# Kernel tuning notes

Hardware: AMD Instinct MI355X
Metric: run time of the kernel (lower is better)

The kernel has to match this reference:

```python
import jax, jax.numpy as jnp
import numpy as np

PRE_NMS_TOPN = 6000   # cfg.TEST.RPN_PRE_NMS_TOP_N
POST_NMS_TOPN = 1000  # cfg.TEST.RPN_POST_NMS_TOP_N
NMS_THRESH = 0.7      # cfg.TEST.RPN_NMS_THRESH
MIN_SIZE = 0.0        # cfg.TEST.RPN_MIN_SIZE
BBOX_XFORM_CLIP = float(np.log(1000.0 / 16.0))
FEAT_STRIDE = 8.0     # 1 / spatial_scale


def _generate_anchors(base_size=16, ratios=(0.5, 1.0, 2.0), scales=(2, 4, 8, 16, 32)):
    """Standard Detectron anchor generation -> (A, 4) = (15, 4)."""
    def whctrs(a):
        w = a[2] - a[0] + 1.0
        h = a[3] - a[1] + 1.0
        return w, h, a[0] + 0.5 * (w - 1.0), a[1] + 0.5 * (h - 1.0)

    def mk(ws, hs, xc, yc):
        ws = ws[:, None]; hs = hs[:, None]
        return np.hstack([xc - 0.5 * (ws - 1.0), yc - 0.5 * (hs - 1.0),
                          xc + 0.5 * (ws - 1.0), yc + 0.5 * (hs - 1.0)])

    base = np.array([0.0, 0.0, base_size - 1.0, base_size - 1.0])
    w, h, xc, yc = whctrs(base)
    rs = np.array(ratios)
    ws = np.round(np.sqrt(w * h / rs))
    hs = np.round(ws * rs)
    ratio_anchors = mk(ws, hs, xc, yc)
    out = []
    for a in ratio_anchors:
        w, h, xc, yc = whctrs(a)
        sc = np.array(scales, dtype=np.float64)
        out.append(mk(w * sc, h * sc, xc, yc))
    return np.vstack(out).astype(np.float32)


def _proposals_one_image(all_anchors, im_info, bbox_deltas, scores):
    # bbox_deltas: (4A, H, W), scores: (A, H, W)
    deltas = bbox_deltas.transpose(1, 2, 0).reshape(-1, 4)  # (K*A, 4)
    s = scores.transpose(1, 2, 0).reshape(-1)               # (K*A,)

    # pre-NMS top-k by objectness (argpartition+argsort in original)
    top_s, order = jax.lax.top_k(s, PRE_NMS_TOPN)
    d = deltas[order]
    anc = all_anchors[order]

    # bbox_transform with weights (1,1,1,1) and dw/dh clipping
    ws = anc[:, 2] - anc[:, 0] + 1.0
    hs = anc[:, 3] - anc[:, 1] + 1.0
    cx = anc[:, 0] + 0.5 * ws
    cy = anc[:, 1] + 0.5 * hs
    dx, dy = d[:, 0], d[:, 1]
    dw = jnp.minimum(d[:, 2], BBOX_XFORM_CLIP)
    dh = jnp.minimum(d[:, 3], BBOX_XFORM_CLIP)
    pcx = dx * ws + cx
    pcy = dy * hs + cy
    pw = jnp.exp(dw) * ws
    ph = jnp.exp(dh) * hs
    x1 = pcx - 0.5 * pw
    y1 = pcy - 0.5 * ph
    x2 = pcx + 0.5 * pw - 1.0
    y2 = pcy + 0.5 * ph - 1.0

    # clip_tiled_boxes to image extent
    h_im, w_im, scale = im_info[0], im_info[1], im_info[2]
    x1 = jnp.clip(x1, 0.0, w_im - 1.0)
    y1 = jnp.clip(y1, 0.0, h_im - 1.0)
    x2 = jnp.clip(x2, 0.0, w_im - 1.0)
    y2 = jnp.clip(y2, 0.0, h_im - 1.0)
    boxes = jnp.stack([x1, y1, x2, y2], axis=1)  # (PRE, 4)

    # _filter_boxes -> validity mask (replaces gather-by-keep)
    bws = x2 - x1 + 1.0
    bhs = y2 - y1 + 1.0
    min_sz = MIN_SIZE * scale
    valid = (bws >= min_sz) & (bhs >= min_sz) & ((x1 + bws / 2.0) < w_im) & ((y1 + bhs / 2.0) < h_im)

    # greedy NMS on score-sorted boxes (boxes already sorted descending)
    areas = bws * bhs
    ix1 = jnp.maximum(x1[:, None], x1[None, :])
    iy1 = jnp.maximum(y1[:, None], y1[None, :])
    ix2 = jnp.minimum(x2[:, None], x2[None, :])
    iy2 = jnp.minimum(y2[:, None], y2[None, :])
    inter = jnp.maximum(ix2 - ix1 + 1.0, 0.0) * jnp.maximum(iy2 - iy1 + 1.0, 0.0)
    iou = inter / (areas[:, None] + areas[None, :] - inter)

    later = jnp.arange(PRE_NMS_TOPN)

    def body(i, keep):
        sup = keep[i] & (iou[i] > NMS_THRESH) & (later > i)
        return keep & ~sup

    keep = jax.lax.fori_loop(0, PRE_NMS_TOPN, body, valid)

    # fixed-size output: top POST_NMS_TOPN surviving boxes, padded (score=-1, box=0)
    masked = jnp.where(keep, top_s, -1.0)
    out_s, idx = jax.lax.top_k(masked, POST_NMS_TOPN)
    pad = (out_s > -1.0).astype(boxes.dtype)
    out_b = boxes[idx] * pad[:, None]
    return out_b, out_s


def reference(rpn_cls_prob, rpn_bbox_pred, im_info, anchors):
    N, A, H, W = rpn_cls_prob.shape
    dt = rpn_bbox_pred.dtype
    shift_x = jnp.arange(W, dtype=dt) * FEAT_STRIDE
    shift_y = jnp.arange(H, dtype=dt) * FEAT_STRIDE
    # torch.meshgrid default 'ij' ordering (faithful to original)
    sx, sy = jnp.meshgrid(shift_x, shift_y, indexing='ij')  # (W, H)
    shifts = jnp.stack([sx.ravel(), sy.ravel(), sx.ravel(), sy.ravel()], axis=1)  # (K, 4)
    all_anchors = (anchors[None, :, :] + shifts[:, None, :]).reshape(-1, 4)  # (K*A, 4)

    boxes, probs = jax.vmap(_proposals_one_image, in_axes=(None, 0, 0, 0))(
        all_anchors, im_info, rpn_bbox_pred, rpn_cls_prob)
    batch_inds = jnp.broadcast_to(jnp.arange(N, dtype=boxes.dtype)[:, None, None],
                                  (N, POST_NMS_TOPN, 1))
    rois = jnp.concatenate([batch_inds, boxes], axis=-1).reshape(-1, 5)
    return rois, probs.reshape(-1)


def setup_inputs() -> dict:
    key = jax.random.key(0)
    k1, k2 = jax.random.split(key)
    N, A, H, W = 2, 15, 128, 128
    rpn_cls_prob = jax.random.uniform(k1, (N, A, H, W), dtype=jnp.float32)
    rpn_bbox_pred = jax.random.normal(k2, (N, 4 * A, H, W), dtype=jnp.float32) * 0.2
    im_info = jnp.tile(jnp.array([[1024.0, 1024.0, 1.0]], dtype=jnp.float32), (N, 1))
    anchors = jnp.asarray(_generate_anchors())
    return {"rpn_cls_prob": rpn_cls_prob, "rpn_bbox_pred": rpn_bbox_pred,
            "im_info": im_info, "anchors": anchors}
```

## Files before the change

kernel.cpp:

```cpp
#include <hip/hip_runtime.h>
#include <hip/hip_bf16.h>

#define A_NUM 15
#define HDIM 128
#define WDIM 128
#define HW (HDIM*WDIM)
#define PER_IMG (A_NUM*HW)
#define NIMG 2
#define PRE_N 6000
#define POST_N 1000
#define NBLK 94
#define NPAD (NBLK*64)
#define SORTN 8192
#define CHUNK4 4096
#define NBIN 16384
#define HPART 16

typedef unsigned long long ull;

#define META_OFF   0u
#define HIST_OFF   64u
#define SEL_OFF    131136u
#define BOX_OFF    262208u
#define VALID_OFF  550976u
#define DIAG_OFF   599104u
#define MASK_OFF   695360u

__device__ __forceinline__ unsigned int f2ord(float f) {
    unsigned int u = __float_as_uint(f);
    return (u & 0x80000000u) ? ~u : (u | 0x80000000u);
}
__device__ __forceinline__ float ord2f(unsigned int u) {
    unsigned int s = (u & 0x80000000u) ? (u ^ 0x80000000u) : ~u;
    return __uint_as_float(s);
}

__global__ __launch_bounds__(1024) void k_hist16(const float* __restrict__ cls,
                                                 unsigned int* __restrict__ hist) {
    __shared__ unsigned int h[NBIN];
    int img = blockIdx.y, part = blockIdx.x;
    int t = threadIdx.x;
    for (int b = t; b < NBIN; b += 1024) h[b] = 0;
    __syncthreads();
    int base = img * PER_IMG + part * (PER_IMG / HPART);
    for (int e = t; e < PER_IMG / HPART; e += 1024) {
        unsigned int u = f2ord(cls[base + e]);
        unsigned int bin = (u >> 16) - 0x8000u;
        if (bin > (NBIN - 1)) bin = NBIN - 1;
        atomicAdd(&h[bin], 1u);
    }
    __syncthreads();
    unsigned int* hp = hist + (size_t)img * NBIN;
    for (int b = t; b < NBIN; b += 1024)
        if (h[b]) atomicAdd(&hp[b], h[b]);
}

__global__ __launch_bounds__(1024) void k_scan16(const unsigned int* __restrict__ hist,
                                                 unsigned int* __restrict__ meta) {
    __shared__ unsigned int csum[1024];
    __shared__ unsigned int aux[64];
    __shared__ unsigned int binv[16];
    int img = blockIdx.x, t = threadIdx.x;
    const unsigned int* hp = hist + (size_t)img * NBIN;
    unsigned int s = 0;
    #pragma unroll
    for (int q = 0; q < 16; ++q) s += hp[t * 16 + q];
    csum[t] = s;
    __syncthreads();
    if (t < 64) {
        unsigned int x = 0;
        #pragma unroll
        for (int q = 0; q < 16; ++q) x += csum[t * 16 + q];
        aux[t] = x;
    }
    __syncthreads();
    if (t < 64) {
        unsigned int suf = 0;
        for (int q = t; q < 64; ++q) suf += aux[q];
        ull mb1 = __ballot(suf >= PRE_N);
        int sstar = 63 - __clzll(mb1);
        unsigned int sufnext = (unsigned)__shfl((int)suf, (sstar + 1) & 63);
        unsigned int cumAbove = (sstar == 63) ? 0u : sufnext;
        unsigned int sufC = 0;
        if (t < 16) {
            for (int q = sstar * 16 + t; q < sstar * 16 + 16; ++q) sufC += csum[q];
            sufC += cumAbove;
        }
        ull mb2 = __ballot((t < 16) && (sufC >= PRE_N));
        int crel = 63 - __clzll(mb2);
        int cstar = sstar * 16 + crel;
        unsigned int cumAbove2 = (crel == 15) ? cumAbove : (unsigned)__shfl((int)sufC, crel + 1);
        if (t < 16) binv[t] = hp[cstar * 16 + t];
        unsigned int sufB = 0;
        if (t < 16) {
            for (int q = t; q < 16; ++q) sufB += binv[q];
            sufB += cumAbove2;
        }
        ull mb3 = __ballot((t < 16) && (sufB >= PRE_N));
        int brel = 63 - __clzll(mb3);
        if (t == 0) {
            meta[2 + img] = (unsigned)(cstar * 16 + brel) + 0x8000u;
            meta[img] = 0u;
        }
    }
}

__global__ __launch_bounds__(256) void k_gather(const float* __restrict__ cls,
                                                unsigned int* __restrict__ meta,
                                                ull* __restrict__ selkeys) {
    __shared__ unsigned int lcnt[NIMG], lbase[NIMG];
    int t = threadIdx.x;
    int tid = blockIdx.x * 256 + t;
    if (t < NIMG) lcnt[t] = 0;
    __syncthreads();
    unsigned int T0 = meta[2], T1 = meta[3];
    int a = tid / HW;
    int pos = tid - a * HW;
    int m = pos * A_NUM + a;
    int lane = t & 63;
    unsigned int uv[NIMG];
    bool pr[NIMG];
    unsigned int lofs[NIMG];
    #pragma unroll
    for (int img = 0; img < NIMG; ++img) {
        unsigned int T = img ? T1 : T0;
        unsigned int u = f2ord(cls[img * PER_IMG + tid]);
        uv[img] = u;
        bool pred = (u >> 16) >= T;
        pr[img] = pred;
        ull mball = __ballot((int)pred);
        unsigned int o = 0;
        if (pred) {
            int leader = __ffsll((long long)mball) - 1;
            unsigned int wbase = 0;
            if (lane == leader) wbase = atomicAdd(&lcnt[img], (unsigned)__popcll(mball));
            wbase = (unsigned)__shfl((int)wbase, leader);
            o = wbase + (unsigned)__popcll(mball & ((1ull << lane) - 1ull));
        }
        lofs[img] = o;
    }
    __syncthreads();
    if (t < NIMG) lbase[t] = atomicAdd(&meta[t], lcnt[t]);
    __syncthreads();
    #pragma unroll
    for (int img = 0; img < NIMG; ++img) {
        if (pr[img]) {
            unsigned int p = lbase[img] + lofs[img];
            if (p < SORTN)
                selkeys[(size_t)img * SORTN + p] =
                    ((ull)(~uv[img]) << 32) | (unsigned int)m;
        }
    }
}

__global__ __launch_bounds__(512) void k_sortA(ull* __restrict__ selkeys,
                                               const unsigned int* __restrict__ meta) {
    __shared__ ull key[CHUNK4];
    int img = blockIdx.x >> 1, c = blockIdx.x & 1;
    unsigned int cnt = meta[img];
    if (cnt > SORTN) cnt = SORTN;
    ull* g = selkeys + (size_t)img * SORTN;
    int base = c * CHUNK4;
    for (int i = threadIdx.x; i < CHUNK4; i += 512)
        key[i] = (base + i < (int)cnt) ? g[base + i] : ~0ull;
    __syncthreads();
    bool desc = (c & 1);
    for (int k = 2; k <= CHUNK4; k <<= 1) {
        for (int j = k >> 1; j > 0; j >>= 1) {
            for (int p = threadIdx.x; p < CHUNK4 / 2; p += 512) {
                int i = ((p & ~(j - 1)) << 1) | (p & (j - 1));
                int x = i | j;
                bool up = (((i & k) == 0) != desc);
                ull A = key[i], B = key[x];
                if ((A > B) == up) { key[i] = B; key[x] = A; }
            }
            __syncthreads();
        }
    }
    for (int i = threadIdx.x; i < CHUNK4; i += 512) g[base + i] = key[i];
}

__global__ __launch_bounds__(512) void k_sortC(ull* __restrict__ selkeys) {
    __shared__ ull key[SORTN];
    int img = blockIdx.x;
    ull* g = selkeys + (size_t)img * SORTN;
    for (int i = threadIdx.x; i < SORTN; i += 512) key[i] = g[i];
    __syncthreads();
    for (int j = SORTN / 2; j > 0; j >>= 1) {
        for (int p = threadIdx.x; p < SORTN / 2; p += 512) {
            int i = ((p & ~(j - 1)) << 1) | (p & (j - 1));
            int x = i | j;
            ull A = key[i], B = key[x];
            if (A > B) { key[i] = B; key[x] = A; }
        }
        __syncthreads();
    }
    for (int i = threadIdx.x; i < PRE_N; i += 512) g[i] = key[i];
}

__global__ void k_decode(const ull* __restrict__ selkeys,
                         const float* __restrict__ bbox, const float* __restrict__ anchors,
                         const float* __restrict__ iminfo,
                         float* __restrict__ boxsoa, unsigned int* __restrict__ validArr) {
    int r = blockIdx.x * blockDim.x + threadIdx.x;
    int img = blockIdx.y;
    if (r >= PRE_N) return;
    ull keyv = selkeys[(size_t)img * SORTN + r];
    unsigned int m = (unsigned int)(keyv & 0xFFFFFFFFu);
    unsigned int u = ~(unsigned int)(keyv >> 32);
    float score = ord2f(u);
    int q = m / A_NUM;
    int a = m - q * A_NUM;
    int w = q & (WDIM - 1);
    int h = q >> 7;
    float sx = (float)h * 8.0f;
    float sy = (float)w * 8.0f;
    float a0 = __fadd_rn(anchors[a * 4 + 0], sx);
    float a1 = __fadd_rn(anchors[a * 4 + 1], sy);
    float a2 = __fadd_rn(anchors[a * 4 + 2], sx);
    float a3 = __fadd_rn(anchors[a * 4 + 3], sy);
    float ws = __fadd_rn(__fsub_rn(a2, a0), 1.0f);
    float hs = __fadd_rn(__fsub_rn(a3, a1), 1.0f);
    float cx = __fadd_rn(a0, __fmul_rn(0.5f, ws));
    float cy = __fadd_rn(a1, __fmul_rn(0.5f, hs));
    const float* bb = bbox + (size_t)img * 4 * A_NUM * HW;
    int base = h * WDIM + w;
    float dx = bb[(a * 4 + 0) * HW + base];
    float dy = bb[(a * 4 + 1) * HW + base];
    float dwv = bb[(a * 4 + 2) * HW + base];
    float dhv = bb[(a * 4 + 3) * HW + base];
    const float CLIPV = 4.135166556742356f;
    float dw = fminf(dwv, CLIPV);
    float dh = fminf(dhv, CLIPV);
    float pcx = __fadd_rn(__fmul_rn(dx, ws), cx);
    float pcy = __fadd_rn(__fmul_rn(dy, hs), cy);
    float pw = __fmul_rn(expf(dw), ws);
    float ph = __fmul_rn(expf(dh), hs);
    float x1 = __fsub_rn(pcx, __fmul_rn(0.5f, pw));
    float y1 = __fsub_rn(pcy, __fmul_rn(0.5f, ph));
    float x2 = __fsub_rn(__fadd_rn(pcx, __fmul_rn(0.5f, pw)), 1.0f);
    float y2 = __fsub_rn(__fadd_rn(pcy, __fmul_rn(0.5f, ph)), 1.0f);
    float him = iminfo[img * 3 + 0], wim = iminfo[img * 3 + 1], scale = iminfo[img * 3 + 2];
    float wmax = __fsub_rn(wim, 1.0f), hmax = __fsub_rn(him, 1.0f);
    x1 = fminf(fmaxf(x1, 0.0f), wmax);
    y1 = fminf(fmaxf(y1, 0.0f), hmax);
    x2 = fminf(fmaxf(x2, 0.0f), wmax);
    y2 = fminf(fmaxf(y2, 0.0f), hmax);
    float bws = __fadd_rn(__fsub_rn(x2, x1), 1.0f);
    float bhs = __fadd_rn(__fsub_rn(y2, y1), 1.0f);
    float minsz = __fmul_rn(0.0f, scale);
    bool valid = (bws >= minsz) && (bhs >= minsz) &&
                 (__fadd_rn(x1, __fdiv_rn(bws, 2.0f)) < wim) &&
                 (__fadd_rn(y1, __fdiv_rn(bhs, 2.0f)) < him);
    float area = __fmul_rn(bws, bhs);
    boxsoa[(0 * NIMG + img) * NPAD + r] = x1;
    boxsoa[(1 * NIMG + img) * NPAD + r] = y1;
    boxsoa[(2 * NIMG + img) * NPAD + r] = x2;
    boxsoa[(3 * NIMG + img) * NPAD + r] = y2;
    boxsoa[(4 * NIMG + img) * NPAD + r] = area;
    boxsoa[(5 * NIMG + img) * NPAD + r] = score;
    validArr[img * NPAD + r] = valid ? 1u : 0u;
}

__global__ __launch_bounds__(256) void k_mask(const float* __restrict__ boxsoa,
                                              ull* __restrict__ M,
                                              ull* __restrict__ diagArr) {
    int jb = blockIdx.x, ibq = blockIdx.y, img = blockIdx.z;
    if (jb < (ibq << 2)) return;
    int t = threadIdx.x, wv = t >> 6, lane = t & 63;
    __shared__ float jx1[64], jy1[64], jx2[64], jy2[64], jar[64];
    const float* X1 = boxsoa + (0 * NIMG + img) * NPAD;
    const float* Y1 = boxsoa + (1 * NIMG + img) * NPAD;
    const float* X2 = boxsoa + (2 * NIMG + img) * NPAD;
    const float* Y2 = boxsoa + (3 * NIMG + img) * NPAD;
    const float* AR = boxsoa + (4 * NIMG + img) * NPAD;
    int j0 = jb * 64;
    if (t < 64) {
        int jidx = j0 + t;
        bool jin = jidx < PRE_N;
        jx1[t] = jin ? X1[jidx] : 0.0f;
        jy1[t] = jin ? Y1[jidx] : 0.0f;
        jx2[t] = jin ? X2[jidx] : 0.0f;
        jy2[t] = jin ? Y2[jidx] : 0.0f;
        jar[t] = jin ? AR[jidx] : 1.0f;
    }
    __syncthreads();
    int ib = ibq * 4 + wv;
    if (ib >= NBLK || jb < ib) return;
    int i = ib * 64 + lane;
    ull bits = 0ULL;
    if (i < PRE_N) {
        float x1 = X1[i], y1 = Y1[i], x2 = X2[i], y2 = Y2[i], ai = AR[i];
        for (int jj = 0; jj < 64; ++jj) {
            int j = j0 + jj;
            if (j == i || j >= PRE_N) continue;
            float ix1 = fmaxf(x1, jx1[jj]);
            float iy1 = fmaxf(y1, jy1[jj]);
            float ix2 = fminf(x2, jx2[jj]);
            float iy2 = fminf(y2, jy2[jj]);
            float iw = fmaxf(__fadd_rn(__fsub_rn(ix2, ix1), 1.0f), 0.0f);
            float ih = fmaxf(__fadd_rn(__fsub_rn(iy2, iy1), 1.0f), 0.0f);
            float inter = __fmul_rn(iw, ih);
            float denom = __fsub_rn(__fadd_rn(ai, jar[jj]), inter);
            float iou = __fdiv_rn(inter, denom);
            if (iou > 0.7f) bits |= (1ULL << jj);
        }
    }
    M[((size_t)img * NPAD + (size_t)i) * NBLK + jb] = bits;
    if (jb == ib) diagArr[(size_t)img * NPAD + i] = bits;
}

__global__ __launch_bounds__(64, 1) void k_reduce(const ull* __restrict__ M_,
                                                  const ull* __restrict__ diagArr,
                                                  const unsigned int* __restrict__ validArr,
                                                  const float* __restrict__ boxsoa,
                                                  float* __restrict__ out) {
    int img = blockIdx.x;
    int t = threadIdx.x;
    __shared__ unsigned short s_list[POST_N];
    const ull* M = M_ + (size_t)img * NPAD * NBLK;
    const ull* D = diagArr + (size_t)img * NPAD;
    const unsigned int* V = validArr + img * NPAD;
    ull d_cur = D[t];
    unsigned int vraw = V[t];
    ull A_acc = 0ULL, tile_cur = 0ULL, keptb_prev = 0ULL;
    int cnt = 0;
    for (int ib = 0; ib < NBLK; ++ib) {
        int cnt_pre = cnt;
        ull a_nx0 = 0, a_nx1 = 0, a_nx2 = 0, a_nx3 = 0, a_nx4 = 0, a_nx5 = 0, a_nx6 = 0, a_nx7 = 0;
        ull a_nx8 = 0, a_nx9 = 0, a_nxA = 0, a_nxB = 0, a_nxC = 0, a_nxD = 0, a_nxE = 0, a_nxF = 0;
        ull tile_nx = 0ULL, d_nx = 0ULL;
        unsigned int v_nx = 0u;
        int col = ib + 1;
        if (col < NBLK) {
            #define AG(reg, u2) { int q = t + (u2 << 6); \
                if (q < cnt_pre) reg = M[(size_t)s_list[q] * NBLK + col]; }
            AG(a_nx0, 0) AG(a_nx1, 1) AG(a_nx2, 2) AG(a_nx3, 3)
            AG(a_nx4, 4) AG(a_nx5, 5) AG(a_nx6, 6) AG(a_nx7, 7)
            AG(a_nx8, 8) AG(a_nx9, 9) AG(a_nxA, 10) AG(a_nxB, 11)
            AG(a_nxC, 12) AG(a_nxD, 13) AG(a_nxE, 14) AG(a_nxF, 15)
            #undef AG
            tile_nx = M[(size_t)(ib * 64 + t) * NBLK + col];
            int i2 = col * 64 + t;
            d_nx = D[i2];
            v_nx = V[i2];
        }
        ull partial = A_acc | (((keptb_prev >> t) & 1ULL) ? tile_cur : 0ULL);
        unsigned int lo = (unsigned)partial, hi = (unsigned)(partial >> 32);
        #pragma unroll
        for (int s2 = 1; s2 < 64; s2 <<= 1) {
            lo |= (unsigned)__shfl_xor((int)lo, s2);
            hi |= (unsigned)__shfl_xor((int)hi, s2);
        }
        ull sup = ((ull)hi << 32) | lo;
        int i = ib * 64 + t;
        bool v_cur = (i < PRE_N) && (vraw != 0u);
        ull validw = __ballot((int)v_cur);
        ull live = validw & ~sup;
        unsigned int dlo = (unsigned)d_cur, dhi = (unsigned)(d_cur >> 32);
        ull keptb = 0ULL;
        while (live) {
            int b = __ffsll((long long)live) - 1;
            keptb |= 1ULL << b;
            if (t == 0) s_list[cnt] = (unsigned short)(ib * 64 + b);
            ++cnt;
            if (cnt >= POST_N) break;
            unsigned int rl = (unsigned)__builtin_amdgcn_readlane((int)dlo, b);
            unsigned int rh = (unsigned)__builtin_amdgcn_readlane((int)dhi, b);
            live &= ~(((ull)rh << 32) | rl);
            live &= ~(1ULL << b);
        }
        if (cnt >= POST_N) break;
        A_acc = (((a_nx0 | a_nx1) | (a_nx2 | a_nx3)) | ((a_nx4 | a_nx5) | (a_nx6 | a_nx7)))
              | (((a_nx8 | a_nx9) | (a_nxA | a_nxB)) | ((a_nxC | a_nxD) | (a_nxE | a_nxF)));
        tile_cur = tile_nx;
        d_cur = d_nx;
        vraw = v_nx;
        keptb_prev = keptb;
    }
    int total = cnt > POST_N ? POST_N : cnt;
    for (int k = t; k < POST_N; k += 64) {
        float x1 = 0.0f, y1 = 0.0f, x2 = 0.0f, y2 = 0.0f, sc = -1.0f;
        if (k < total) {
            int r = (int)s_list[k];
            x1 = boxsoa[(0 * NIMG + img) * NPAD + r];
            y1 = boxsoa[(1 * NIMG + img) * NPAD + r];
            x2 = boxsoa[(2 * NIMG + img) * NPAD + r];
            y2 = boxsoa[(3 * NIMG + img) * NPAD + r];
            sc = boxsoa[(5 * NIMG + img) * NPAD + r];
        }
        float* roi = out + (size_t)(img * POST_N + k) * 5;
        roi[0] = (float)img;
        roi[1] = x1;
        roi[2] = y1;
        roi[3] = x2;
        roi[4] = y2;
        out[NIMG * POST_N * 5 + img * POST_N + k] = sc;
    }
}

extern "C" void kernel_launch(void* const* d_in, const int* in_sizes, int n_in,
                              void* d_out, int out_size, void* d_ws, size_t ws_size,
                              hipStream_t stream) {
    const float* cls = (const float*)d_in[0];
    const float* bbox = (const float*)d_in[1];
    const float* iminfo = (const float*)d_in[2];
    const float* anchors = (const float*)d_in[3];
    float* out = (float*)d_out;
    char* ws = (char*)d_ws;

    unsigned int* meta = (unsigned int*)(ws + META_OFF);
    unsigned int* hist = (unsigned int*)(ws + HIST_OFF);
    ull* selkeys = (ull*)(ws + SEL_OFF);
    float* boxsoa = (float*)(ws + BOX_OFF);
    unsigned int* validArr = (unsigned int*)(ws + VALID_OFF);
    ull* diagArr = (ull*)(ws + DIAG_OFF);
    ull* mask = (ull*)(ws + MASK_OFF);

    hipMemsetAsync(hist, 0, (size_t)NIMG * NBIN * sizeof(unsigned int), stream);
    k_hist16<<<dim3(HPART, NIMG), 1024, 0, stream>>>(cls, hist);
    k_scan16<<<NIMG, 1024, 0, stream>>>(hist, meta);
    k_gather<<<PER_IMG / 256, 256, 0, stream>>>(cls, meta, selkeys);
    k_sortA<<<2 * NIMG, 512, 0, stream>>>(selkeys, meta);
    k_sortC<<<NIMG, 512, 0, stream>>>(selkeys);
    k_decode<<<dim3((PRE_N + 255) / 256, NIMG), 256, 0, stream>>>(selkeys, bbox, anchors, iminfo,
                                                                  boxsoa, validArr);
    k_mask<<<dim3(NBLK, (NBLK + 3) / 4, NIMG), 256, 0, stream>>>(boxsoa, mask, diagArr);
    k_reduce<<<NIMG, 64, 0, stream>>>(mask, diagArr, validArr, boxsoa, out);
}
```

Measured before the change: 292.9 us.

## Store NMS mask column-major and OR suppression via per-lane kept bitmaps

```diff
diff --git a/kernel.cpp b/kernel.cpp
--- a/kernel.cpp
+++ b/kernel.cpp
@@ -263,10 +263,10 @@
 }
 
 __global__ __launch_bounds__(256) void k_mask(const float* __restrict__ boxsoa,
-                                              ull* __restrict__ M,
+                                              ull* __restrict__ Mc,
                                               ull* __restrict__ diagArr) {
-    int jb = blockIdx.x, ibq = blockIdx.y, img = blockIdx.z;
-    if (jb < (ibq << 2)) return;
+    int cb = blockIdx.x, rbq = blockIdx.y, img = blockIdx.z;
+    if ((rbq << 2) > cb) return;
     int t = threadIdx.x, wv = t >> 6, lane = t & 63;
     __shared__ float jx1[64], jy1[64], jx2[64], jy2[64], jar[64];
     const float* X1 = boxsoa + (0 * NIMG + img) * NPAD;
@@ -274,7 +274,7 @@
     const float* X2 = boxsoa + (2 * NIMG + img) * NPAD;
     const float* Y2 = boxsoa + (3 * NIMG + img) * NPAD;
     const float* AR = boxsoa + (4 * NIMG + img) * NPAD;
-    int j0 = jb * 64;
+    int j0 = cb * 64;
     if (t < 64) {
         int jidx = j0 + t;
         bool jin = jidx < PRE_N;
@@ -285,15 +285,15 @@
         jar[t] = jin ? AR[jidx] : 1.0f;
     }
     __syncthreads();
-    int ib = ibq * 4 + wv;
-    if (ib >= NBLK || jb < ib) return;
-    int i = ib * 64 + lane;
+    int rb = rbq * 4 + wv;
+    if (rb > cb) return;
+    int r = rb * 64 + lane;
     ull bits = 0ULL;
-    if (i < PRE_N) {
-        float x1 = X1[i], y1 = Y1[i], x2 = X2[i], y2 = Y2[i], ai = AR[i];
+    if (r < PRE_N) {
+        float x1 = X1[r], y1 = Y1[r], x2 = X2[r], y2 = Y2[r], ai = AR[r];
         for (int jj = 0; jj < 64; ++jj) {
             int j = j0 + jj;
-            if (j == i || j >= PRE_N) continue;
+            if (j == r || j >= PRE_N) continue;
             float ix1 = fmaxf(x1, jx1[jj]);
             float iy1 = fmaxf(y1, jy1[jj]);
             float ix2 = fminf(x2, jx2[jj]);
@@ -306,11 +306,11 @@
             if (iou > 0.7f) bits |= (1ULL << jj);
         }
     }
-    M[((size_t)img * NPAD + (size_t)i) * NBLK + jb] = bits;
-    if (jb == ib) diagArr[(size_t)img * NPAD + i] = bits;
-}
-
-__global__ __launch_bounds__(64, 1) void k_reduce(const ull* __restrict__ M_,
+    Mc[((size_t)img * NBLK + cb) * NPAD + r] = bits;
+    if (rb == cb) diagArr[(size_t)img * NPAD + r] = bits;
+}
+
+__global__ __launch_bounds__(64, 1) void k_reduce(const ull* __restrict__ Mc,
                                                   const ull* __restrict__ diagArr,
                                                   const unsigned int* __restrict__ validArr,
                                                   const float* __restrict__ boxsoa,
@@ -318,35 +318,31 @@
     int img = blockIdx.x;
     int t = threadIdx.x;
     __shared__ unsigned short s_list[POST_N];
-    const ull* M = M_ + (size_t)img * NPAD * NBLK;
+    const ull* MC = Mc + (size_t)img * NBLK * NPAD;
     const ull* D = diagArr + (size_t)img * NPAD;
     const unsigned int* V = validArr + img * NPAD;
     ull d_cur = D[t];
     unsigned int vraw = V[t];
-    ull A_acc = 0ULL, tile_cur = 0ULL, keptb_prev = 0ULL;
+    ull kTlo = 0ULL, kThi = 0ULL;
+    ull acc_cur = 0ULL;
     int cnt = 0;
     for (int ib = 0; ib < NBLK; ++ib) {
-        int cnt_pre = cnt;
-        ull a_nx0 = 0, a_nx1 = 0, a_nx2 = 0, a_nx3 = 0, a_nx4 = 0, a_nx5 = 0, a_nx6 = 0, a_nx7 = 0;
-        ull a_nx8 = 0, a_nx9 = 0, a_nxA = 0, a_nxB = 0, a_nxC = 0, a_nxD = 0, a_nxE = 0, a_nxF = 0;
-        ull tile_nx = 0ULL, d_nx = 0ULL;
+        int col = ib + 1;
+        bool doload = col < NBLK;
+        const ull* Mcol = MC + (size_t)col * NPAD;
+        ull val[NBLK];
+        #pragma unroll
+        for (int u = 0; u < NBLK; ++u) {
+            if (u <= ib && doload) val[u] = Mcol[u * 64 + t];
+            else val[u] = 0ULL;
+        }
+        ull d_nx = 0ULL;
         unsigned int v_nx = 0u;
-        int col = ib + 1;
-        if (col < NBLK) {
-            #define AG(reg, u2) { int q = t + (u2 << 6); \
-                if (q < cnt_pre) reg = M[(size_t)s_list[q] * NBLK + col]; }
-            AG(a_nx0, 0) AG(a_nx1, 1) AG(a_nx2, 2) AG(a_nx3, 3)
-            AG(a_nx4, 4) AG(a_nx5, 5) AG(a_nx6, 6) AG(a_nx7, 7)
-            AG(a_nx8, 8) AG(a_nx9, 9) AG(a_nxA, 10) AG(a_nxB, 11)
-            AG(a_nxC, 12) AG(a_nxD, 13) AG(a_nxE, 14) AG(a_nxF, 15)
-            #undef AG
-            tile_nx = M[(size_t)(ib * 64 + t) * NBLK + col];
-            int i2 = col * 64 + t;
-            d_nx = D[i2];
-            v_nx = V[i2];
-        }
-        ull partial = A_acc | (((keptb_prev >> t) & 1ULL) ? tile_cur : 0ULL);
-        unsigned int lo = (unsigned)partial, hi = (unsigned)(partial >> 32);
+        if (doload) {
+            d_nx = D[col * 64 + t];
+            v_nx = V[col * 64 + t];
+        }
+        unsigned int lo = (unsigned)acc_cur, hi = (unsigned)(acc_cur >> 32);
         #pragma unroll
         for (int s2 = 1; s2 < 64; s2 <<= 1) {
             lo |= (unsigned)__shfl_xor((int)lo, s2);
@@ -371,12 +367,19 @@
             live &= ~(1ULL << b);
         }
         if (cnt >= POST_N) break;
-        A_acc = (((a_nx0 | a_nx1) | (a_nx2 | a_nx3)) | ((a_nx4 | a_nx5) | (a_nx6 | a_nx7)))
-              | (((a_nx8 | a_nx9) | (a_nxA | a_nxB)) | ((a_nxC | a_nxD) | (a_nxE | a_nxF)));
-        tile_cur = tile_nx;
+        ull mybit = (keptb >> t) & 1ULL;
+        if (ib < 64) kTlo |= mybit << ib;
+        else kThi |= mybit << (ib - 64);
+        ull accN = 0ULL;
+        #pragma unroll
+        for (int u = 0; u < NBLK; ++u) {
+            if (u > 93) continue;
+            ull mu = (u < 64) ? ((kTlo >> u) & 1ULL) : ((kThi >> (u - 64)) & 1ULL);
+            accN |= mu ? val[u] : 0ULL;
+        }
+        acc_cur = accN;
         d_cur = d_nx;
         vraw = v_nx;
-        keptb_prev = keptb;
     }
     int total = cnt > POST_N ? POST_N : cnt;
     for (int k = t; k < POST_N; k += 64) {
```

Result: slower. 307.1 us (+4.8%).
